# Kernel optimization log

Hardware: AMD Instinct MI355X
Metric: run time of the kernel (lower is better)

## Reference

```python
import jax, jax.numpy as jnp
import numpy as np

N_HEAD = 16
N_KV = 4
HEAD_DIM = 128
EPS = 1e-6


def setup_inputs() -> dict:
    key = jax.random.key(0)
    k1, k2, k3 = jax.random.split(key, 3)
    d_model = N_HEAD * HEAD_DIM
    qkv_out = (N_HEAD + 2 * N_KV) * HEAD_DIM
    B, T = 2, 2048
    x = jax.random.normal(k1, (B, T, d_model), dtype=jnp.float32)
    W_qkv = jax.random.normal(k2, (d_model, qkv_out), dtype=jnp.float32) * (d_model ** -0.5)
    W_proj = jax.random.normal(k3, (d_model, d_model), dtype=jnp.float32) * (d_model ** -0.5)
    q_scale = jnp.ones((HEAD_DIM,), dtype=jnp.float32)
    k_scale = jnp.ones((HEAD_DIM,), dtype=jnp.float32)
    return {"x": x, "W_qkv": W_qkv, "W_proj": W_proj, "q_scale": q_scale, "k_scale": k_scale}


def _rms_norm(t):
    return t * jax.lax.rsqrt(jnp.mean(t * t, axis=-1, keepdims=True) + EPS)


def reference(x, W_qkv, W_proj, q_scale, k_scale):
    B, T, C = x.shape
    qkv = x @ W_qkv  # [B, T, (H+2*KV)*D]
    q, k, v = jnp.split(qkv, [N_HEAD * HEAD_DIM, (N_HEAD + N_KV) * HEAD_DIM], axis=-1)
    q = q.reshape(B, T, N_HEAD, HEAD_DIM).transpose(0, 2, 1, 3)  # [B,H,T,D]
    k = k.reshape(B, T, N_KV, HEAD_DIM).transpose(0, 2, 1, 3)    # [B,KV,T,D]
    v = v.reshape(B, T, N_KV, HEAD_DIM).transpose(0, 2, 1, 3)
    # QK RMS-norm with learned per-dim scales
    q = _rms_norm(q) * q_scale
    k = _rms_norm(k) * k_scale
    # GQA: repeat kv heads to match query heads
    rep = N_HEAD // N_KV
    k = jnp.repeat(k, rep, axis=1)
    v = jnp.repeat(v, rep, axis=1)
    # causal SDPA
    scale = 1.0 / jnp.sqrt(jnp.float32(HEAD_DIM))
    scores = jnp.einsum('bhqd,bhkd->bhqk', q, k) * scale
    causal = jnp.tril(jnp.ones((T, T), dtype=bool))
    scores = jnp.where(causal, scores, jnp.finfo(scores.dtype).min)
    attn = jax.nn.softmax(scores, axis=-1)
    y = jnp.einsum('bhqk,bhkd->bhqd', attn, v)  # [B,H,T,D]
    y = y.transpose(0, 2, 1, 3).reshape(B, T, C)
    return y @ W_proj
```

## Files before the change

kernel.cpp:

```cpp
#include <hip/hip_runtime.h>

typedef __bf16 bf16;
typedef __bf16 bf16x8 __attribute__((ext_vector_type(8)));
typedef __bf16 bf16x4 __attribute__((ext_vector_type(4)));
typedef float f32x4 __attribute__((ext_vector_type(4)));
typedef float f32x16 __attribute__((ext_vector_type(16)));
typedef unsigned u32x4 __attribute__((ext_vector_type(4)));

#define EXP2F(x) __builtin_amdgcn_exp2f(x)

#define LOAD_LDS16(gp, lp)                                                     \
  __builtin_amdgcn_global_load_lds(                                            \
      (const __attribute__((address_space(1))) void*)(gp),                     \
      (__attribute__((address_space(3))) void*)(lp), 16, 0, 0)

__global__ __launch_bounds__(256) void k_pre(const float* __restrict__ x,
                                             const float* __restrict__ Wqkv,
                                             const float* __restrict__ Wproj,
                                             bf16* __restrict__ xb,
                                             bf16* __restrict__ Wqkvt,
                                             bf16* __restrict__ Wprojt) {
  int bid = blockIdx.x, tid = threadIdx.x;
  if (bid < 8192) {
    int i = bid * 256 + tid;
    float4 v = ((const float4*)x)[i];
    bf16x4 o = {(bf16)v.x, (bf16)v.y, (bf16)v.z, (bf16)v.w};
    ((bf16x4*)xb)[i] = o;
    return;
  }
  __shared__ bf16 t[64 * 65];
  const float* in;
  bf16* out;
  int R, C, c0, r0;
  if (bid < 9728) {
    int f = bid - 8192;
    in = Wqkv; out = Wqkvt; R = 2048; C = 3072;
    c0 = (f % 48) * 64; r0 = (f / 48) * 64;
  } else {
    int f = bid - 9728;
    in = Wproj; out = Wprojt; R = 2048; C = 2048;
    c0 = (f & 31) * 64; r0 = (f >> 5) * 64;
  }
#pragma unroll
  for (int i = 0; i < 16; ++i) {
    int f = i * 256 + tid;
    int rl = f >> 6, cl = f & 63;
    t[rl * 65 + cl] = (bf16)in[(size_t)(r0 + rl) * C + c0 + cl];
  }
  __syncthreads();
#pragma unroll
  for (int i = 0; i < 16; ++i) {
    int f = i * 256 + tid;
    int cl = f >> 6, rl = f & 63;
    out[(size_t)(c0 + cl) * R + r0 + rl] = t[rl * 65 + cl];
  }
}

template <typename OutT, int BM>
__global__ __launch_bounds__(512, 2) void k_gemm256(const bf16* __restrict__ A,
                                                    const bf16* __restrict__ Bt,
                                                    OutT* __restrict__ C,
                                                    int M, int N, int K) {
  constexpr int ASZ = 4 * BM * 8;
  constexpr int MREP = BM / 32;
  __shared__ alignas(16) bf16 As[2][2][ASZ];
  __shared__ alignas(16) bf16 Bs[2][2][4 * 256 * 8];
  int tid = threadIdx.x;
  int wid = tid >> 6, lane = tid & 63;
  int g = lane >> 4, lr = lane & 15;
  int wrow = (wid >> 2) * (BM / 2), wcol = (wid & 3) * 64;
  int gx = gridDim.x;
  int flat = blockIdx.y * gx + blockIdx.x;
  int cpx = (gx * gridDim.y) >> 3;
  int f2 = (flat & 7) * cpx + (flat >> 3);
  int row0 = (f2 % gx) * BM, col0 = (f2 / gx) * 256;
  int NT = K >> 6;
  f32x4 acc[MREP][4] = {};

  auto stageA = [&](int buf, int kh, int kt) {
#pragma unroll
    for (int pass = 0; pass < BM / 128; ++pass) {
      int slot = pass * 512 + tid;
      int kseg, row;
      if constexpr (BM == 256) { kseg = slot >> 8; row = slot & 255; }
      else { kseg = slot >> 7; row = slot & 127; }
      LOAD_LDS16(A + (size_t)(row0 + row) * K + kt * 64 + kh * 32 + kseg * 8,
                 &As[buf][kh][slot * 8]);
    }
  };
  auto stageB = [&](int buf, int kh, int kt) {
#pragma unroll
    for (int pass = 0; pass < 2; ++pass) {
      int slot = pass * 512 + tid;
      int kseg = slot >> 8, row = slot & 255;
      LOAD_LDS16(Bt + (size_t)(col0 + row) * K + kt * 64 + kh * 32 + kseg * 8,
                 &Bs[buf][kh][slot * 8]);
    }
  };
  auto dsA = [&](int buf, int s, int mq, bf16x8* af) {
#pragma unroll
    for (int i = 0; i < 4; ++i)
      af[i] = *(const bf16x8*)&As[buf][s]
                  [(g * BM + wrow + (mq * 4 + i) * 16 + lr) * 8];
  };
  auto dsB = [&](int buf, int s, bf16x8* bfr) {
#pragma unroll
    for (int i = 0; i < 4; ++i)
      bfr[i] = *(const bf16x8*)&Bs[buf][s][((g << 8) + wcol + i * 16 + lr) * 8];
  };
  auto mfma16 = [&](int mq, bf16x8* af, bf16x8* bfr) {
    __builtin_amdgcn_s_setprio(1);
#pragma unroll
    for (int i = 0; i < 4; ++i)
#pragma unroll
      for (int n = 0; n < 4; ++n)
        acc[mq * 4 + i][n] = __builtin_amdgcn_mfma_f32_16x16x32_bf16(
            af[i], bfr[n], acc[mq * 4 + i][n], 0, 0, 0);
    __builtin_amdgcn_s_setprio(0);
  };

  stageA(0, 0, 0);
  stageB(0, 0, 0);
  stageA(0, 1, 0);
  stageB(0, 1, 0);
  if constexpr (BM == 256)
    asm volatile("s_waitcnt vmcnt(4)" ::: "memory");
  else
    asm volatile("s_waitcnt vmcnt(3)" ::: "memory");
  __builtin_amdgcn_s_barrier();

  for (int T = 0; T < NT; ++T) {
    int buf = T & 1, nbuf = buf ^ 1;
    bool more = (T + 1 < NT);
    bf16x8 af[4], bfr[4];
    if constexpr (BM == 256) {
      dsA(buf, 0, 0, af);
      dsB(buf, 0, bfr);
      if (more) stageA(nbuf, 0, T + 1);
      __builtin_amdgcn_s_barrier();
      mfma16(0, af, bfr);
      __builtin_amdgcn_s_barrier();
      dsA(buf, 0, 1, af);
      if (more) {
        stageB(nbuf, 0, T + 1);
        asm volatile("s_waitcnt vmcnt(4)" ::: "memory");
      } else {
        asm volatile("s_waitcnt vmcnt(0)" ::: "memory");
      }
      __builtin_amdgcn_s_barrier();
      mfma16(1, af, bfr);
      __builtin_amdgcn_s_barrier();
      dsA(buf, 1, 0, af);
      dsB(buf, 1, bfr);
      if (more) stageA(nbuf, 1, T + 1);
      __builtin_amdgcn_s_barrier();
      mfma16(0, af, bfr);
      __builtin_amdgcn_s_barrier();
      dsA(buf, 1, 1, af);
      if (more) {
        stageB(nbuf, 1, T + 1);
        asm volatile("s_waitcnt vmcnt(4)" ::: "memory");
      }
      __builtin_amdgcn_s_barrier();
      mfma16(1, af, bfr);
      __builtin_amdgcn_s_barrier();
    } else {
      dsA(buf, 0, 0, af);
      dsB(buf, 0, bfr);
      if (more) {
        stageA(nbuf, 0, T + 1);
        stageB(nbuf, 0, T + 1);
        asm volatile("s_waitcnt vmcnt(3)" ::: "memory");
      } else {
        asm volatile("s_waitcnt vmcnt(0)" ::: "memory");
      }
      __builtin_amdgcn_s_barrier();
      mfma16(0, af, bfr);
      __builtin_amdgcn_s_barrier();
      dsA(buf, 1, 0, af);
      dsB(buf, 1, bfr);
      if (more) {
        stageA(nbuf, 1, T + 1);
        stageB(nbuf, 1, T + 1);
        asm volatile("s_waitcnt vmcnt(3)" ::: "memory");
      }
      __builtin_amdgcn_s_barrier();
      mfma16(0, af, bfr);
      __builtin_amdgcn_s_barrier();
    }
  }

#pragma unroll
  for (int mi = 0; mi < MREP; ++mi)
#pragma unroll
    for (int ni = 0; ni < 4; ++ni) {
      int rb = row0 + wrow + mi * 16 + g * 4;
      int cc = col0 + wcol + ni * 16 + lr;
#pragma unroll
      for (int r = 0; r < 4; ++r) C[(size_t)(rb + r) * N + cc] = (OutT)acc[mi][ni][r];
    }
}

__global__ __launch_bounds__(256) void k_post(bf16* __restrict__ qkv,
                                              const float* __restrict__ qs,
                                              const float* __restrict__ ks,
                                              bf16* __restrict__ Vt) {
  int bid = blockIdx.x, tid = threadIdx.x;
  if (bid < 4096) {
    int tok = bid;
    int wid = tid >> 6, lane = tid & 63;
    int d = lane * 2;
    bf16* rowp = qkv + (size_t)tok * 3072;
#pragma unroll
    for (int i = 0; i < 5; ++i) {
      int cb = (i < 4) ? (wid + i * 4) * 128 : 2048 + wid * 128;
      float v0 = (float)rowp[cb + d], v1 = (float)rowp[cb + d + 1];
      float ss = v0 * v0 + v1 * v1;
#pragma unroll
      for (int off = 1; off < 64; off <<= 1) ss += __shfl_xor(ss, off);
      float r = rsqrtf(ss * (1.0f / 128.0f) + 1e-6f);
      float s0, s1, extra;
      if (i < 4) {
        s0 = qs[d]; s1 = qs[d + 1];
        extra = 0.08838834764831845f * 1.4426950408889634f;
      } else {
        s0 = ks[d]; s1 = ks[d + 1]; extra = 1.0f;
      }
      rowp[cb + d] = (bf16)(v0 * r * s0 * extra);
      rowp[cb + d + 1] = (bf16)(v1 * r * s1 * extra);
    }
    return;
  }
  __shared__ bf16 t[64 * 65];
  int f = bid - 4096;
  int t0 = (f & 31) * 64;
  int d0 = ((f >> 5) & 1) * 64;
  int bh = f >> 6;
  int b = bh >> 2, kvh = bh & 3;
  const bf16* src = qkv + (size_t)(b * 2048) * 3072 + 2560 + kvh * 128;
  bf16* dst = Vt + (size_t)bh * 262144 + (size_t)(t0 >> 6) * 8192;
#pragma unroll
  for (int i = 0; i < 16; ++i) {
    int ff = i * 256 + tid;
    int tl = ff >> 6, dl = ff & 63;
    t[tl * 65 + dl] = src[(size_t)(t0 + tl) * 3072 + d0 + dl];
  }
  __syncthreads();
#pragma unroll
  for (int i = 0; i < 2; ++i) {
    int v = i * 256 + tid;
    int c = v >> 6, dv = v & 63;
    bf16x8 o;
#pragma unroll
    for (int j = 0; j < 8; ++j) o[j] = t[(c * 8 + j) * 65 + dv];
    *(bf16x8*)&dst[(size_t)c * 1024 + (size_t)(d0 + dv) * 8] = o;
  }
}

__device__ inline unsigned pack2bf(float a, float b) {
  union { bf16 h[2]; unsigned u; } x;
  x.h[0] = (bf16)a;
  x.h[1] = (bf16)b;
  return x.u;
}

__global__ __launch_bounds__(256, 2) void k_attn(const bf16* __restrict__ qkv,
                                                 const bf16* __restrict__ Vt,
                                                 bf16* __restrict__ y) {
  int flat = blockIdx.x;
  int slot = flat >> 8;
  int j = flat & 255;
  int xcd = j & 7, iw = j >> 3;
  int h = xcd + 8 * (iw & 1);
  int r = iw >> 1;
  int b = r & 1;
  int qt = slot ? (r >> 1) : (15 - (r >> 1));
  int kvh = h >> 2;
  int tid = threadIdx.x;
  int wid = tid >> 6, lane = tid & 63;
  int qc = lane & 31, hi = lane >> 5;
  __shared__ alignas(16) bf16 Ks[2][16 * 64 * 8];
  __shared__ alignas(16) bf16 Vs[2][8 * 128 * 8];
  const bf16* Qb = qkv + (size_t)(b * 2048) * 3072 + h * 128;
  const bf16* Kb = qkv + (size_t)(b * 2048) * 3072 + 2048 + kvh * 128;
  const bf16* Vb = Vt + (size_t)(b * 4 + kvh) * 262144;
  int qw0 = qt * 128 + wid * 32;
  int qg = qw0 + qc;
  bf16x8 qf[8];
#pragma unroll
  for (int s = 0; s < 8; ++s)
    qf[s] = *(const bf16x8*)&Qb[(size_t)qg * 3072 + s * 16 + hi * 8];
  f32x16 acc[4] = {};
  float mrun = -1e30f, lrun = 0.f;

  auto STAGE = [&](int buf, int kt2) {
    int s0 = kt2 * 64;
#pragma unroll
    for (int i = 0; i < 4; ++i) {
      int sl = i * 256 + tid;
      int ch = sl >> 6, row = sl & 63;
      LOAD_LDS16(Kb + (size_t)(s0 + row) * 3072 + ch * 8, &Ks[buf][sl * 8]);
    }
#pragma unroll
    for (int i = 0; i < 4; ++i) {
      int sl = i * 256 + tid;
      LOAD_LDS16(Vb + (size_t)kt2 * 8192 + sl * 8, &Vs[buf][sl * 8]);
    }
  };

  STAGE(0, 0);
  int cur = 0;
  int ktmax = 2 * qt + 1;
  for (int kt = 0; kt <= ktmax; ++kt) {
    int s0 = kt * 64;
    if (kt < ktmax) {
      STAGE(cur ^ 1, kt + 1);
      asm volatile("s_waitcnt vmcnt(8)" ::: "memory");
    } else {
      asm volatile("s_waitcnt vmcnt(0)" ::: "memory");
    }
    __builtin_amdgcn_s_barrier();
    __builtin_amdgcn_sched_barrier(0);
    if (s0 <= qw0 + 31) {
      f32x16 sc[2] = {};
      __builtin_amdgcn_s_setprio(1);
#pragma unroll
      for (int s = 0; s < 8; ++s)
#pragma unroll
        for (int n = 0; n < 2; ++n) {
          bf16x8 kf =
              *(const bf16x8*)&Ks[cur][(((2 * s + hi) << 6) + n * 32 + qc) * 8];
          sc[n] =
              __builtin_amdgcn_mfma_f32_32x32x16_bf16(kf, qf[s], sc[n], 0, 0, 0);
        }
      __builtin_amdgcn_s_setprio(0);
      if (s0 + 63 > qw0) {
#pragma unroll
        for (int n = 0; n < 2; ++n)
#pragma unroll
          for (int r2 = 0; r2 < 16; ++r2) {
            int kg = s0 + n * 32 + (r2 & 3) + 8 * (r2 >> 2) + 4 * hi;
            if (kg > qg) sc[n][r2] = -1e30f;
          }
      }
      float pm = -1e30f;
#pragma unroll
      for (int n = 0; n < 2; ++n)
#pragma unroll
        for (int r2 = 0; r2 < 16; ++r2) pm = fmaxf(pm, sc[n][r2]);
      pm = fmaxf(pm, __shfl_xor(pm, 32));
      if (__any(pm > mrun + 11.0f)) {
        float mnew = fmaxf(mrun, pm);
        float scl = EXP2F(mrun - mnew);
        mrun = mnew;
        lrun *= scl;
        float sv[16];
#pragma unroll
        for (int r2 = 0; r2 < 16; ++r2)
          sv[r2] = __shfl(scl, (r2 & 3) + 8 * (r2 >> 2) + 4 * hi);
#pragma unroll
        for (int dt = 0; dt < 4; ++dt)
#pragma unroll
          for (int r2 = 0; r2 < 16; ++r2) acc[dt][r2] *= sv[r2];
      }
      float rs = 0.f;
#pragma unroll
      for (int n = 0; n < 2; ++n) {
        unsigned pk[8];
#pragma unroll
        for (int mm = 0; mm < 8; ++mm) {
          float e0 = EXP2F(sc[n][2 * mm] - mrun);
          float e1 = EXP2F(sc[n][2 * mm + 1] - mrun);
          rs += e0 + e1;
          pk[mm] = pack2bf(e0, e1);
        }
#pragma unroll
        for (int l2 = 0; l2 < 2; ++l2) {
          unsigned a0 = pk[4 * l2 + 0], b0 = pk[4 * l2 + 2];
          unsigned a1 = pk[4 * l2 + 1], b1 = pk[4 * l2 + 3];
          asm volatile("v_permlane32_swap_b32 %0, %1" : "+v"(a0), "+v"(b0));
          asm volatile("v_permlane32_swap_b32 %0, %1" : "+v"(a1), "+v"(b1));
          u32x4 w = {a0, a1, b0, b1};
          bf16x8 pf = __builtin_bit_cast(bf16x8, w);
          int c = 2 * (2 * n + l2) + hi;
          __builtin_amdgcn_s_setprio(1);
#pragma unroll
          for (int dt = 0; dt < 4; ++dt) {
            bf16x8 vf =
                *(const bf16x8*)&Vs[cur][((c << 7) + dt * 32 + qc) * 8];
            acc[dt] =
                __builtin_amdgcn_mfma_f32_32x32x16_bf16(pf, vf, acc[dt], 0, 0, 0);
          }
          __builtin_amdgcn_s_setprio(0);
        }
      }
      rs += __shfl_xor(rs, 32);
      lrun += rs;
    }
    __builtin_amdgcn_sched_barrier(0);
    __builtin_amdgcn_s_barrier();
    cur ^= 1;
  }
  float rlv = 1.0f / lrun;
  float rcl[16];
#pragma unroll
  for (int r2 = 0; r2 < 16; ++r2)
    rcl[r2] = __shfl(rlv, (r2 & 3) + 8 * (r2 >> 2) + 4 * hi);
#pragma unroll
  for (int dt = 0; dt < 4; ++dt)
#pragma unroll
    for (int r2 = 0; r2 < 16; ++r2) {
      int row = qw0 + (r2 & 3) + 8 * (r2 >> 2) + 4 * hi;
      float v = acc[dt][r2] * rcl[r2];
      y[(size_t)(b * 2048 + row) * 2048 + h * 128 + dt * 32 + qc] = (bf16)v;
    }
}

extern "C" void kernel_launch(void* const* d_in, const int* in_sizes, int n_in,
                              void* d_out, int out_size, void* d_ws,
                              size_t ws_size, hipStream_t stream) {
  const float* x = (const float*)d_in[0];
  const float* Wqkv = (const float*)d_in[1];
  const float* Wproj = (const float*)d_in[2];
  const float* qs = (const float*)d_in[3];
  const float* ks = (const float*)d_in[4];
  float* out = (float*)d_out;
  char* ws = (char*)d_ws;

  bf16* xb = (bf16*)(ws);
  bf16* Wqkvt = (bf16*)(ws + (size_t)(16u << 20));
  bf16* Wprojt = (bf16*)(ws + (size_t)(28u << 20));
  bf16* qkv = (bf16*)(ws + (size_t)(36u << 20));
  bf16* Vt = Wqkvt;
  bf16* y = xb;

  k_pre<<<10752, 256, 0, stream>>>(x, Wqkv, Wproj, xb, Wqkvt, Wprojt);
  k_gemm256<bf16, 256><<<dim3(16, 12), 512, 0, stream>>>(xb, Wqkvt, qkv, 4096, 3072, 2048);
  k_post<<<4608, 256, 0, stream>>>(qkv, qs, ks, Vt);
  k_attn<<<dim3(512, 1, 1), 256, 0, stream>>>(qkv, Vt, y);
  k_gemm256<float, 128><<<dim3(32, 8), 512, 0, stream>>>(y, Wprojt, out, 4096, 2048, 2048);
}
```

Measured before the change: 246.6 us.

## Fuse QK RMS-norm and scaling into the QKV GEMM epilogue

Moves the per-head RMS normalization of Q and K (with learned scales and the softmax log2 scale) into the epilogue of the QKV projection GEMM. Each 256-column tile covers two heads, and row sums of squares are reduced across waves through shared memory. This removes the separate read-modify-write pass over the Q/K part of the qkv buffer, so k_post now only does the V transpose. The cost is extra shared memory, a block barrier and some epilogue arithmetic in the GEMM, which could affect occupancy.

```diff
diff --git a/kernel.cpp b/kernel.cpp
--- a/kernel.cpp
+++ b/kernel.cpp
@@ -56,11 +56,13 @@
   }
 }
 
-template <typename OutT, int BM>
+template <typename OutT, int BM, bool QKN>
 __global__ __launch_bounds__(512, 2) void k_gemm256(const bf16* __restrict__ A,
                                                     const bf16* __restrict__ Bt,
                                                     OutT* __restrict__ C,
-                                                    int M, int N, int K) {
+                                                    int M, int N, int K,
+                                                    const float* __restrict__ qs,
+                                                    const float* __restrict__ ks) {
   constexpr int ASZ = 4 * BM * 8;
   constexpr int MREP = BM / 32;
   __shared__ alignas(16) bf16 As[2][2][ASZ];
@@ -190,6 +192,46 @@
     }
   }
 
+  if constexpr (QKN) {
+    __shared__ float part[256][4];
+#pragma unroll
+    for (int mi = 0; mi < MREP; ++mi)
+#pragma unroll
+      for (int r = 0; r < 4; ++r) {
+        float s = 0.f;
+#pragma unroll
+        for (int ni = 0; ni < 4; ++ni) {
+          float v = acc[mi][ni][r];
+          s += v * v;
+        }
+#pragma unroll
+        for (int off = 1; off < 16; off <<= 1) s += __shfl_xor(s, off);
+        if (lr == 0)
+          part[(wid >> 2) * 128 + mi * 16 + g * 4 + r][wid & 3] = s;
+      }
+    __syncthreads();
+    int hidx = (col0 >> 7) + ((wid & 3) >> 1);
+    if (hidx < 20) {
+#pragma unroll
+      for (int mi = 0; mi < MREP; ++mi)
+#pragma unroll
+        for (int ni = 0; ni < 4; ++ni) {
+          int d = (wid & 1) * 64 + ni * 16 + lr;
+          float scl = (hidx < 16)
+              ? qs[d] * (0.08838834764831845f * 1.4426950408889634f)
+              : ks[d];
+#pragma unroll
+          for (int r = 0; r < 4; ++r) {
+            int rl = (wid >> 2) * 128 + mi * 16 + g * 4 + r;
+            int hp = (wid & 3) >> 1;
+            float ss = part[rl][hp * 2] + part[rl][hp * 2 + 1];
+            float rms = rsqrtf(ss * (1.0f / 128.0f) + 1e-6f);
+            acc[mi][ni][r] *= rms * scl;
+          }
+        }
+    }
+  }
+
 #pragma unroll
   for (int mi = 0; mi < MREP; ++mi)
 #pragma unroll
@@ -201,38 +243,11 @@
     }
 }
 
-__global__ __launch_bounds__(256) void k_post(bf16* __restrict__ qkv,
-                                              const float* __restrict__ qs,
-                                              const float* __restrict__ ks,
+__global__ __launch_bounds__(256) void k_post(const bf16* __restrict__ qkv,
                                               bf16* __restrict__ Vt) {
-  int bid = blockIdx.x, tid = threadIdx.x;
-  if (bid < 4096) {
-    int tok = bid;
-    int wid = tid >> 6, lane = tid & 63;
-    int d = lane * 2;
-    bf16* rowp = qkv + (size_t)tok * 3072;
-#pragma unroll
-    for (int i = 0; i < 5; ++i) {
-      int cb = (i < 4) ? (wid + i * 4) * 128 : 2048 + wid * 128;
-      float v0 = (float)rowp[cb + d], v1 = (float)rowp[cb + d + 1];
-      float ss = v0 * v0 + v1 * v1;
-#pragma unroll
-      for (int off = 1; off < 64; off <<= 1) ss += __shfl_xor(ss, off);
-      float r = rsqrtf(ss * (1.0f / 128.0f) + 1e-6f);
-      float s0, s1, extra;
-      if (i < 4) {
-        s0 = qs[d]; s1 = qs[d + 1];
-        extra = 0.08838834764831845f * 1.4426950408889634f;
-      } else {
-        s0 = ks[d]; s1 = ks[d + 1]; extra = 1.0f;
-      }
-      rowp[cb + d] = (bf16)(v0 * r * s0 * extra);
-      rowp[cb + d + 1] = (bf16)(v1 * r * s1 * extra);
-    }
-    return;
-  }
   __shared__ bf16 t[64 * 65];
-  int f = bid - 4096;
+  int tid = threadIdx.x;
+  int f = blockIdx.x;
   int t0 = (f & 31) * 64;
   int d0 = ((f >> 5) & 1) * 64;
   int bh = f >> 6;
@@ -435,8 +450,10 @@
   bf16* y = xb;
 
   k_pre<<<10752, 256, 0, stream>>>(x, Wqkv, Wproj, xb, Wqkvt, Wprojt);
-  k_gemm256<bf16, 256><<<dim3(16, 12), 512, 0, stream>>>(xb, Wqkvt, qkv, 4096, 3072, 2048);
-  k_post<<<4608, 256, 0, stream>>>(qkv, qs, ks, Vt);
+  k_gemm256<bf16, 256, true><<<dim3(16, 12), 512, 0, stream>>>(
+      xb, Wqkvt, qkv, 4096, 3072, 2048, qs, ks);
+  k_post<<<512, 256, 0, stream>>>(qkv, Vt);
   k_attn<<<dim3(512, 1, 1), 256, 0, stream>>>(qkv, Vt, y);
-  k_gemm256<float, 128><<<dim3(32, 8), 512, 0, stream>>>(y, Wprojt, out, 4096, 2048, 2048);
-}
+  k_gemm256<float, 128, false><<<dim3(32, 8), 512, 0, stream>>>(
+      y, Wprojt, out, 4096, 2048, 2048, nullptr, nullptr);
+}
```

Measured after the change: 249.2 us. No clear change (+1.0%).

## Move Wproj transpose into idle extra blocks of QKV GEMM and vectorize pre-pass

Applied to the files above, without the earlier changes.

The Wproj fp32-to-bf16 transpose is taken out of the pre-pass kernel and handled by 64 extra blocks appended to the QKV GEMM grid (192 tiles to 256 blocks), so it runs on CUs that the 192-tile GEMM leaves idle. The x conversion now processes 8 elements per thread, and the transpose write-out uses 4-wide bf16 stores. The aim is a shorter pre-pass and hiding the Wproj conversion behind the GEMM, at the cost of extra blocks competing for bandwidth and the shared-memory budget in the GEMM launch.

```diff
diff --git a/kernel.cpp b/kernel.cpp
--- a/kernel.cpp
+++ b/kernel.cpp
@@ -16,43 +16,36 @@
 
 __global__ __launch_bounds__(256) void k_pre(const float* __restrict__ x,
                                              const float* __restrict__ Wqkv,
-                                             const float* __restrict__ Wproj,
                                              bf16* __restrict__ xb,
-                                             bf16* __restrict__ Wqkvt,
-                                             bf16* __restrict__ Wprojt) {
+                                             bf16* __restrict__ Wqkvt) {
   int bid = blockIdx.x, tid = threadIdx.x;
-  if (bid < 8192) {
+  if (bid < 4096) {
     int i = bid * 256 + tid;
-    float4 v = ((const float4*)x)[i];
-    bf16x4 o = {(bf16)v.x, (bf16)v.y, (bf16)v.z, (bf16)v.w};
-    ((bf16x4*)xb)[i] = o;
+    float4 v0 = ((const float4*)x)[2 * i];
+    float4 v1 = ((const float4*)x)[2 * i + 1];
+    bf16x8 o = {(bf16)v0.x, (bf16)v0.y, (bf16)v0.z, (bf16)v0.w,
+                (bf16)v1.x, (bf16)v1.y, (bf16)v1.z, (bf16)v1.w};
+    ((bf16x8*)xb)[i] = o;
     return;
   }
   __shared__ bf16 t[64 * 65];
-  const float* in;
-  bf16* out;
-  int R, C, c0, r0;
-  if (bid < 9728) {
-    int f = bid - 8192;
-    in = Wqkv; out = Wqkvt; R = 2048; C = 3072;
-    c0 = (f % 48) * 64; r0 = (f / 48) * 64;
-  } else {
-    int f = bid - 9728;
-    in = Wproj; out = Wprojt; R = 2048; C = 2048;
-    c0 = (f & 31) * 64; r0 = (f >> 5) * 64;
-  }
+  int f = bid - 4096;
+  int c0 = (f % 48) * 64, r0 = (f / 48) * 64;
+  const int C = 3072, R = 2048;
 #pragma unroll
   for (int i = 0; i < 16; ++i) {
-    int f = i * 256 + tid;
-    int rl = f >> 6, cl = f & 63;
-    t[rl * 65 + cl] = (bf16)in[(size_t)(r0 + rl) * C + c0 + cl];
+    int f2 = i * 256 + tid;
+    int rl = f2 >> 6, cl = f2 & 63;
+    t[rl * 65 + cl] = (bf16)Wqkv[(size_t)(r0 + rl) * C + c0 + cl];
   }
   __syncthreads();
 #pragma unroll
-  for (int i = 0; i < 16; ++i) {
-    int f = i * 256 + tid;
-    int cl = f >> 6, rl = f & 63;
-    out[(size_t)(c0 + cl) * R + r0 + rl] = t[rl * 65 + cl];
+  for (int i = 0; i < 4; ++i) {
+    int idx = i * 256 + tid;
+    int cl = idx >> 4, rl0 = (idx & 15) * 4;
+    bf16x4 o = {t[(rl0 + 0) * 65 + cl], t[(rl0 + 1) * 65 + cl],
+                t[(rl0 + 2) * 65 + cl], t[(rl0 + 3) * 65 + cl]};
+    *(bf16x4*)&Wqkvt[(size_t)(c0 + cl) * R + r0 + rl0] = o;
   }
 }
 
@@ -60,7 +53,9 @@
 __global__ __launch_bounds__(512, 2) void k_gemm256(const bf16* __restrict__ A,
                                                     const bf16* __restrict__ Bt,
                                                     OutT* __restrict__ C,
-                                                    int M, int N, int K) {
+                                                    int M, int N, int K,
+                                                    const float* __restrict__ Wp,
+                                                    bf16* __restrict__ Wpt) {
   constexpr int ASZ = 4 * BM * 8;
   constexpr int MREP = BM / 32;
   __shared__ alignas(16) bf16 As[2][2][ASZ];
@@ -71,7 +66,33 @@
   int wrow = (wid >> 2) * (BM / 2), wcol = (wid & 3) * 64;
   int gx = gridDim.x;
   int flat = blockIdx.y * gx + blockIdx.x;
-  int cpx = (gx * gridDim.y) >> 3;
+  int ntiles = (M / BM) * (N / 256);
+  if (flat >= ntiles) {
+    bf16* t = (bf16*)&As[0][0][0];
+    int b2 = flat - ntiles;
+    for (int k = 0; k < 16; ++k) {
+      int st = b2 * 16 + k;
+      int c0 = (st & 31) * 64, r0 = (st >> 5) * 64;
+#pragma unroll
+      for (int i = 0; i < 8; ++i) {
+        int f2 = i * 512 + tid;
+        int rl = f2 >> 6, cl = f2 & 63;
+        t[rl * 65 + cl] = (bf16)Wp[(size_t)(r0 + rl) * 2048 + c0 + cl];
+      }
+      __syncthreads();
+#pragma unroll
+      for (int i = 0; i < 2; ++i) {
+        int idx = i * 512 + tid;
+        int cl = idx >> 4, rl0 = (idx & 15) * 4;
+        bf16x4 o = {t[(rl0 + 0) * 65 + cl], t[(rl0 + 1) * 65 + cl],
+                    t[(rl0 + 2) * 65 + cl], t[(rl0 + 3) * 65 + cl]};
+        *(bf16x4*)&Wpt[(size_t)(c0 + cl) * 2048 + r0 + rl0] = o;
+      }
+      __syncthreads();
+    }
+    return;
+  }
+  int cpx = ntiles >> 3;
   int f2 = (flat & 7) * cpx + (flat >> 3);
   int row0 = (f2 % gx) * BM, col0 = (f2 / gx) * 256;
   int NT = K >> 6;
@@ -434,9 +455,11 @@
   bf16* Vt = Wqkvt;
   bf16* y = xb;
 
-  k_pre<<<10752, 256, 0, stream>>>(x, Wqkv, Wproj, xb, Wqkvt, Wprojt);
-  k_gemm256<bf16, 256><<<dim3(16, 12), 512, 0, stream>>>(xb, Wqkvt, qkv, 4096, 3072, 2048);
+  k_pre<<<5632, 256, 0, stream>>>(x, Wqkv, xb, Wqkvt);
+  k_gemm256<bf16, 256><<<dim3(16, 16), 512, 0, stream>>>(
+      xb, Wqkvt, qkv, 4096, 3072, 2048, Wproj, Wprojt);
   k_post<<<4608, 256, 0, stream>>>(qkv, qs, ks, Vt);
   k_attn<<<dim3(512, 1, 1), 256, 0, stream>>>(qkv, Vt, y);
-  k_gemm256<float, 128><<<dim3(32, 8), 512, 0, stream>>>(y, Wprojt, out, 4096, 2048, 2048);
-}
+  k_gemm256<float, 128><<<dim3(32, 8), 512, 0, stream>>>(
+      y, Wprojt, out, 4096, 2048, 2048, nullptr, nullptr);
+}
```

After: 242.4 us. About the same (-1.7%).
